# Kernel tuning notes

Hardware: AMD Instinct MI355X
Metric: run time of the kernel (lower is better)

## Reference

```python
import jax, jax.numpy as jnp
import numpy as np

B, S, E, H, D = 1, 2048, 1024, 16, 64
LAM_INIT = 0.8  # \u03bbinit from init_kwargs
LN_EPS = 1e-5


def setup_inputs() -> dict:
    key = jax.random.key(0)
    ks = jax.random.split(key, 6)
    w = 0.02  # weight init scale
    return {
        "X": jax.random.normal(ks[0], (B, S, E), dtype=jnp.float32),
        "Wq": jax.random.normal(ks[1], (H, E, 2 * D), dtype=jnp.float32) * w,
        "bq": jnp.zeros((H, 2 * D), dtype=jnp.float32),
        "Wk": jax.random.normal(ks[2], (H, E, 2 * D), dtype=jnp.float32) * w,
        "bk": jnp.zeros((H, 2 * D), dtype=jnp.float32),
        "Wv": jax.random.normal(ks[3], (H, E, D), dtype=jnp.float32) * w,
        "bv": jnp.zeros((H, D), dtype=jnp.float32),
        "Wo": jax.random.normal(ks[4], (H * D, E), dtype=jnp.float32) * w,
        "bo": jnp.zeros((E,), dtype=jnp.float32),
        "gamma": jnp.ones((E,), dtype=jnp.float32),
        "beta": jnp.zeros((E,), dtype=jnp.float32),
        "lam": jnp.float32(0.5),
    }


def reference(X, Wq, bq, Wk, bk, Wv, bv, Wo, bo, gamma, beta, lam):
    # Batched over heads: Q,K -> [B,H,S,2D], V -> [B,H,S,D]
    Q = jnp.einsum("bse,hec->bhsc", X, Wq) + bq[None, :, None, :]
    K = jnp.einsum("bse,hec->bhsc", X, Wk) + bk[None, :, None, :]
    V = jnp.einsum("bse,hed->bhsd", X, Wv) + bv[None, :, None, :]
    d = Wv.shape[-1]
    Q1, Q2 = Q[..., :d], Q[..., d:]
    K1, K2 = K[..., :d], K[..., d:]
    s = 1.0 / jnp.sqrt(jnp.float32(d))
    A1 = jnp.einsum("bhqd,bhkd->bhqk", Q1, K1) * s
    A2 = jnp.einsum("bhqd,bhkd->bhqk", Q2, K2) * s
    P = jax.nn.softmax(A1, axis=-1) - lam * jax.nn.softmax(A2, axis=-1)
    O = jnp.einsum("bhqk,bhkd->bhqd", P, V)  # [B,H,S,D]
    Ocat = jnp.transpose(O, (0, 2, 1, 3)).reshape(O.shape[0], O.shape[2], -1)  # [B,S,H*D]
    Y = Ocat @ Wo + bo
    mu = jnp.mean(Y, axis=-1, keepdims=True)
    var = jnp.var(Y, axis=-1, keepdims=True)
    Yn = (Y - mu) * jax.lax.rsqrt(var + LN_EPS) * gamma + beta
    return Yn * (1.0 - LAM_INIT)
```

## Files before the change

kernel.cpp:

```cpp
#include <hip/hip_runtime.h>

#define S_LEN 2048
#define EDIM  1024
#define HEADS 16
#define DHEAD 64

typedef __attribute__((ext_vector_type(8))) short bf16x8;
typedef __attribute__((ext_vector_type(4))) short short4v;
typedef __attribute__((ext_vector_type(4))) float f32x4;

__device__ inline unsigned short f2bf(float f) {
    unsigned int u = __float_as_uint(f);
    unsigned int r = (u + 0x7FFFu + ((u >> 16) & 1u)) >> 16;
    return (unsigned short)r;
}
__device__ inline float bf2f(unsigned short b) {
    return __uint_as_float(((unsigned int)b) << 16);
}
__device__ inline void load_lds16(const void* g, void* l) {
    __builtin_amdgcn_global_load_lds(
        (const __attribute__((address_space(1))) unsigned int*)g,
        (__attribute__((address_space(3))) unsigned int*)l, 16, 0, 0);
}

__global__ void k_convert_x(const float* __restrict__ x, short* __restrict__ xb, int n4) {
    int i = blockIdx.x * blockDim.x + threadIdx.x;
    if (i >= n4) return;
    f32x4 v = ((const f32x4*)x)[i];
    short4v o;
    o[0] = (short)f2bf(v[0]); o[1] = (short)f2bf(v[1]);
    o[2] = (short)f2bf(v[2]); o[3] = (short)f2bf(v[3]);
    ((short4v*)xb)[i] = o;
}

__global__ void k_transpose_cvt(const float* __restrict__ in, short* __restrict__ out, int R, int C) {
    __shared__ float tile[32][33];
    const int b = blockIdx.z;
    in  += (size_t)b * R * C;
    out += (size_t)b * R * C;
    const int c0 = blockIdx.x * 32, r0 = blockIdx.y * 32;
    #pragma unroll
    for (int yy = 0; yy < 4; ++yy) {
        int r = r0 + threadIdx.y + yy * 8, c = c0 + threadIdx.x;
        tile[threadIdx.y + yy * 8][threadIdx.x] = (r < R && c < C) ? in[(size_t)r * C + c] : 0.f;
    }
    __syncthreads();
    #pragma unroll
    for (int yy = 0; yy < 4; ++yy) {
        int c = c0 + threadIdx.y + yy * 8, r = r0 + threadIdx.x;
        if (c < C && r < R) out[(size_t)c * R + r] = (short)f2bf(tile[threadIdx.x][threadIdx.y + yy * 8]);
    }
}

template<int BM, int BN, int WR, int WC>
__device__ inline void gemm_core(const char* Ag, int ldaB, const char* Bg, int ldbB,
                                 int K, char* sA, char* sB, f32x4* acc) {
    constexpr int FM = BM / (WR * 16), FN = BN / (WC * 16);
    constexpr int RA = BM / 32, RB = BN / 32;
    const int lane = threadIdx.x & 63, wave = threadIdx.x >> 6;
    const int rl = lane & 15, g = lane >> 4;
    const int wrow = (wave / WC) * (BM / WR);
    const int wcol = (wave % WC) * (BN / WC);
    const int lr = lane >> 3;
    const int lc = ((lane & 7) ^ lr) << 4;
    const char* aSrc = Ag + (size_t)(wave * 8 + lr) * ldaB + lc;
    const char* bSrc = Bg + (size_t)(wave * 8 + lr) * ldbB + lc;

    for (int t = 0; t < K / 64; ++t) {
        __syncthreads();
        #pragma unroll
        for (int i = 0; i < RA; ++i)
            load_lds16(aSrc + (size_t)t * 128 + (size_t)i * 32 * ldaB, sA + (i * 4 + wave) * 1024);
        #pragma unroll
        for (int i = 0; i < RB; ++i)
            load_lds16(bSrc + (size_t)t * 128 + (size_t)i * 32 * ldbB, sB + (i * 4 + wave) * 1024);
        __syncthreads();
        #pragma unroll
        for (int kk = 0; kk < 2; ++kk) {
            bf16x8 af[FM], bf[FN];
            #pragma unroll
            for (int f = 0; f < FM; ++f) {
                const int r = wrow + f * 16 + rl;
                af[f] = *(const bf16x8*)(sA + r * 128 + (((kk * 4 + g) ^ (r & 7)) << 4));
            }
            #pragma unroll
            for (int j = 0; j < FN; ++j) {
                const int r = wcol + j * 16 + rl;
                bf[j] = *(const bf16x8*)(sB + r * 128 + (((kk * 4 + g) ^ (r & 7)) << 4));
            }
            #pragma unroll
            for (int f = 0; f < FM; ++f)
                #pragma unroll
                for (int j = 0; j < FN; ++j)
                    acc[f * FN + j] = __builtin_amdgcn_mfma_f32_16x16x32_bf16(af[f], bf[j], acc[f * FN + j], 0, 0, 0);
        }
    }
}

__global__ __launch_bounds__(256) void k_gemm_qkv(
        const short* __restrict__ Xb,
        const short* __restrict__ WqT, const short* __restrict__ WkT, const short* __restrict__ WvT,
        const float* __restrict__ bq, const float* __restrict__ bk, const float* __restrict__ bv,
        short* __restrict__ Qh, short* __restrict__ Kh, short* __restrict__ Vt) {
    __shared__ __align__(16) char sA[16384], sB[16384];
    int id = blockIdx.x;
    id = (id & 7) * 80 + (id >> 3);
    const int mbase = (id % 16) * 128;
    const int y = id / 16;

    const short* Bt; const float* bias; int nbase; int which;
    if (y < 16)      { which = 0; Bt = WqT; bias = bq; nbase = y * 128; }
    else if (y < 32) { which = 1; Bt = WkT; bias = bk; nbase = (y - 16) * 128; }
    else             { which = 2; Bt = WvT; bias = bv; nbase = (y - 32) * 128; }

    f32x4 acc[16];
    #pragma unroll
    for (int i = 0; i < 16; ++i) acc[i] = (f32x4){0.f, 0.f, 0.f, 0.f};

    gemm_core<128, 128, 2, 2>((const char*)Xb + (size_t)mbase * 2048, 2048,
                              (const char*)Bt + (size_t)nbase * 2048, 2048,
                              EDIM, sA, sB, acc);

    const int lane = threadIdx.x & 63, wave = threadIdx.x >> 6;
    const int wr = (wave >> 1) * 64, wc = (wave & 1) * 64;
    const int rl = lane & 15, g = lane >> 4;
    const float qscale = 0.125f * 1.44269504088896f;
    #pragma unroll
    for (int i = 0; i < 4; ++i)
        #pragma unroll
        for (int j = 0; j < 4; ++j)
            #pragma unroll
            for (int jj = 0; jj < 4; ++jj) {
                int s = mbase + wr + i * 16 + g * 4 + jj;
                int n = nbase + wc + j * 16 + rl;
                float v = acc[i * 4 + j][jj] + bias[n];
                if (which == 0) v *= qscale;
                short b16 = (short)f2bf(v);
                if (which == 0)      Qh[((size_t)(n >> 7) * S_LEN + s) * 128 + (n & 127)] = b16;
                else if (which == 1) Kh[((size_t)(n >> 7) * S_LEN + s) * 128 + (n & 127)] = b16;
                else                 Vt[(size_t)n * S_LEN + s] = b16;
            }
}

__global__ __launch_bounds__(256) void k_attn(
        const short* __restrict__ Qh, const short* __restrict__ Kh,
        const short* __restrict__ Vt, const float* __restrict__ lam_p,
        short* __restrict__ Ocat) {
    __shared__ __align__(16) char smem[65536];
    char* Kl = smem;
    char* Vl = smem + 32768;
    char* Pl = smem + 49152;

    const int lane = threadIdx.x & 63, wave = threadIdx.x >> 6;
    const int rl = lane & 15, g = lane >> 4;
    const int h = blockIdx.y;
    const int qbase = blockIdx.x * 64 + wave * 16;
    const int swz = (rl & 7) << 4;
    const int kx = rl & 7;

    const char* Kgb = (const char*)(Kh + (size_t)h * S_LEN * 128);
    const char* Vgb = (const char*)(Vt + (size_t)h * DHEAD * S_LEN);
    const short* Qp = Qh + (size_t)h * S_LEN * 128;
    char* Pb0 = Pl + wave * 4096;
    char* Pb1 = Pb0 + 2048;

    const int kofs0 = (lane >> 4) * 256 + (((lane & 15) ^ (lane >> 4)) << 4);
    const int kofs1 = (lane >> 4) * 256 + (((lane & 15) ^ ((lane >> 4) + 4)) << 4);
    const int vofs  = (lane >> 3) * 4096 + (((lane & 7) ^ (lane >> 3)) << 4);

    bf16x8 qf[2][2];
    #pragma unroll
    for (int p = 0; p < 2; ++p)
        #pragma unroll
        for (int kc = 0; kc < 2; ++kc)
            qf[p][kc] = *(const bf16x8*)&Qp[(size_t)(qbase + rl) * 128 + p * 64 + kc * 32 + g * 8];

    #pragma unroll
    for (int cc = 0; cc < 4; ++cc) {
        int c = wave * 4 + cc;
        load_lds16(Kgb + c * 1024 + ((cc & 1) ? kofs1 : kofs0), Kl + c * 1024);
    }
    #pragma unroll
    for (int cc = 0; cc < 2; ++cc) {
        int c = wave * 2 + cc;
        load_lds16(Vgb + (size_t)c * 32768 + vofs, Vl + c * 1024);
    }

    f32x4 acc[2][4];
    float m[2], l[2];
    #pragma unroll
    for (int p = 0; p < 2; ++p) {
        #pragma unroll
        for (int t = 0; t < 4; ++t) acc[p][t] = (f32x4){0.f, 0.f, 0.f, 0.f};
        m[p] = 0.f; l[p] = 0.f;
    }

    __syncthreads();

    const int NIT = S_LEN / 64;
    for (int it = 0; it < NIT; ++it) {
        const int cur = it & 1;
        if (it + 1 < NIT) {
            const size_t nkv = (size_t)(it + 1) * 64;
            char* kb = Kl + (cur ^ 1) * 16384;
            char* vb = Vl + (cur ^ 1) * 8192;
            #pragma unroll
            for (int cc = 0; cc < 4; ++cc) {
                int c = wave * 4 + cc;
                load_lds16(Kgb + nkv * 256 + c * 1024 + ((cc & 1) ? kofs1 : kofs0), kb + c * 1024);
            }
            #pragma unroll
            for (int cc = 0; cc < 2; ++cc) {
                int c = wave * 2 + cc;
                load_lds16(Vgb + (size_t)c * 32768 + nkv * 2 + vofs, vb + c * 1024);
            }
        }
        const char* kb = Kl + cur * 16384;
        const char* vb = Vl + cur * 8192;

        f32x4 sc[2][4];
        #pragma unroll
        for (int t = 0; t < 4; ++t) {
            #pragma unroll
            for (int p = 0; p < 2; ++p) {
                f32x4 z = (f32x4){0.f, 0.f, 0.f, 0.f};
                #pragma unroll
                for (int kc = 0; kc < 2; ++kc) {
                    bf16x8 kf = *(const bf16x8*)(kb + t * 4096 + rl * 256 + (((p * 8 + kc * 4 + g) ^ kx) << 4));
                    z = __builtin_amdgcn_mfma_f32_16x16x32_bf16(kf, qf[p][kc], z, 0, 0, 0);
                }
                sc[p][t] = z;
            }
        }

        float bm[2];
        #pragma unroll
        for (int p = 0; p < 2; ++p) {
            float mx = sc[p][0][0];
            #pragma unroll
            for (int t = 0; t < 4; ++t)
                #pragma unroll
                for (int jj = 0; jj < 4; ++jj)
                    mx = fmaxf(mx, sc[p][t][jj]);
            mx = fmaxf(mx, __shfl_xor(mx, 16, 64));
            mx = fmaxf(mx, __shfl_xor(mx, 32, 64));
            bm[p] = mx;
        }

        if (it == 0) {
            m[0] = bm[0]; m[1] = bm[1];
        } else if (!__all((bm[0] <= m[0] + 8.f) && (bm[1] <= m[1] + 8.f))) {
            #pragma unroll
            for (int p = 0; p < 2; ++p) {
                float mn = fmaxf(m[p], bm[p]);
                float fac = exp2f(m[p] - mn);
                l[p] *= fac; m[p] = mn;
                #pragma unroll
                for (int jj = 0; jj < 4; ++jj) {
                    float fq = __shfl(fac, g * 4 + jj, 64);
                    #pragma unroll
                    for (int t = 0; t < 4; ++t) acc[p][t][jj] *= fq;
                }
            }
        }

        #pragma unroll
        for (int p = 0; p < 2; ++p) {
            char* Pb = p ? Pb1 : Pb0;
            float rs = 0.f;
            #pragma unroll
            for (int t = 0; t < 4; ++t) {
                #pragma unroll
                for (int jjp = 0; jjp < 4; jjp += 2) {
                    float e0 = exp2f(sc[p][t][jjp]     - m[p]);
                    float e1 = exp2f(sc[p][t][jjp + 1] - m[p]);
                    rs += e0 + e1;
                    unsigned u;
                    asm("v_cvt_pk_bf16_f32 %0, %1, %2" : "=v"(u) : "v"(e0), "v"(e1));
                    *(unsigned*)(Pb + rl * 128 + (((t * 16 + g * 4 + jjp) * 2) ^ swz)) = u;
                }
            }
            rs += __shfl_xor(rs, 16, 64);
            rs += __shfl_xor(rs, 32, 64);
            l[p] += rs;
        }

        #pragma unroll
        for (int kc = 0; kc < 2; ++kc) {
            bf16x8 pa0 = *(const bf16x8*)(Pb0 + rl * 128 + ((kc * 64 + g * 16) ^ swz));
            bf16x8 pa1 = *(const bf16x8*)(Pb1 + rl * 128 + ((kc * 64 + g * 16) ^ swz));
            #pragma unroll
            for (int t = 0; t < 4; ++t) {
                bf16x8 vf = *(const bf16x8*)(vb + t * 2048 + rl * 128 + (((kc * 4 + g) ^ kx) << 4));
                acc[0][t] = __builtin_amdgcn_mfma_f32_16x16x32_bf16(pa0, vf, acc[0][t], 0, 0, 0);
                acc[1][t] = __builtin_amdgcn_mfma_f32_16x16x32_bf16(pa1, vf, acc[1][t], 0, 0, 0);
            }
        }
        __syncthreads();
    }

    const float lam = lam_p[0];
    float inv0[4], inv1[4];
    #pragma unroll
    for (int jj = 0; jj < 4; ++jj) {
        inv0[jj] = 1.0f / __shfl(l[0], g * 4 + jj, 64);
        inv1[jj] = lam  / __shfl(l[1], g * 4 + jj, 64);
    }
    #pragma unroll
    for (int t = 0; t < 4; ++t)
        #pragma unroll
        for (int jj = 0; jj < 4; ++jj) {
            float o = acc[0][t][jj] * inv0[jj] - acc[1][t][jj] * inv1[jj];
            int s = qbase + g * 4 + jj;
            Ocat[(size_t)s * 1024 + h * 64 + t * 16 + rl] = (short)f2bf(o);
        }
}

__global__ __launch_bounds__(256) void k_gemm_out(
        const short* __restrict__ Ocat, const short* __restrict__ WoT,
        const float* __restrict__ bo, float* __restrict__ Yws) {
    __shared__ __align__(16) char sA[8192], sB[16384];
    int id = blockIdx.x;
    id = (id & 7) * 32 + (id >> 3);
    const int mbase = (id % 32) * 64;
    const int nbase = (id / 32) * 128;

    f32x4 acc[8];
    #pragma unroll
    for (int i = 0; i < 8; ++i) acc[i] = (f32x4){0.f, 0.f, 0.f, 0.f};

    gemm_core<64, 128, 1, 4>((const char*)Ocat + (size_t)mbase * 2048, 2048,
                             (const char*)WoT + (size_t)nbase * 2048, 2048,
                             1024, sA, sB, acc);

    const int lane = threadIdx.x & 63, wave = threadIdx.x >> 6;
    const int rl = lane & 15, g = lane >> 4;
    #pragma unroll
    for (int f = 0; f < 4; ++f)
        #pragma unroll
        for (int j = 0; j < 2; ++j)
            #pragma unroll
            for (int jj = 0; jj < 4; ++jj) {
                int s = mbase + f * 16 + g * 4 + jj;
                int e = nbase + wave * 32 + j * 16 + rl;
                Yws[(size_t)s * 1024 + e] = acc[f * 2 + j][jj] + bo[e];
            }
}

__global__ __launch_bounds__(256) void k_ln(
        const float* __restrict__ Yws, const float* __restrict__ gamma,
        const float* __restrict__ beta, float* __restrict__ out) {
    const int s = blockIdx.x;
    const int tid = threadIdx.x;
    f32x4 y = ((const f32x4*)(Yws + (size_t)s * 1024))[tid];
    float sum = y[0] + y[1] + y[2] + y[3];
    float sq  = y[0]*y[0] + y[1]*y[1] + y[2]*y[2] + y[3]*y[3];
    #pragma unroll
    for (int off = 1; off < 64; off <<= 1) {
        sum += __shfl_xor(sum, off, 64);
        sq  += __shfl_xor(sq,  off, 64);
    }
    __shared__ float ls[2][4];
    const int wave = tid >> 6, lane = tid & 63;
    if (lane == 0) { ls[0][wave] = sum; ls[1][wave] = sq; }
    __syncthreads();
    sum = ls[0][0] + ls[0][1] + ls[0][2] + ls[0][3];
    sq  = ls[1][0] + ls[1][1] + ls[1][2] + ls[1][3];
    const float mu = sum * (1.f / 1024.f);
    const float var = sq * (1.f / 1024.f) - mu * mu;
    const float rstd = rsqrtf(var + 1e-5f);
    f32x4 gg = ((const f32x4*)gamma)[tid];
    f32x4 bb = ((const f32x4*)beta)[tid];
    f32x4 o;
    #pragma unroll
    for (int k = 0; k < 4; ++k)
        o[k] = ((y[k] - mu) * rstd * gg[k] + bb[k]) * 0.2f;
    ((f32x4*)(out + (size_t)s * 1024))[tid] = o;
}

extern "C" void kernel_launch(void* const* d_in, const int* in_sizes, int n_in,
                              void* d_out, int out_size, void* d_ws, size_t ws_size,
                              hipStream_t stream) {
    const float* X     = (const float*)d_in[0];
    const float* Wq    = (const float*)d_in[1];
    const float* bq    = (const float*)d_in[2];
    const float* Wk    = (const float*)d_in[3];
    const float* bk    = (const float*)d_in[4];
    const float* Wv    = (const float*)d_in[5];
    const float* bv    = (const float*)d_in[6];
    const float* Wo    = (const float*)d_in[7];
    const float* bo    = (const float*)d_in[8];
    const float* gamma = (const float*)d_in[9];
    const float* beta  = (const float*)d_in[10];
    const float* lam   = (const float*)d_in[11];
    float* out = (float*)d_out;

    char* ws = (char*)d_ws;
    const size_t MB = 1u << 20;
    short* Xb  = (short*)(ws + 0);
    short* WqT = (short*)(ws + 4 * MB);
    short* WkT = (short*)(ws + 8 * MB);
    short* WvT = (short*)(ws + 12 * MB);
    short* WoT = (short*)(ws + 14 * MB);
    short* Qh  = (short*)(ws + 16 * MB);
    short* Kh  = (short*)(ws + 24 * MB);
    short* Vt  = (short*)(ws + 32 * MB);
    short* Oc  = (short*)(ws + 36 * MB);
    float* Yws = (float*)(ws + 0);

    k_convert_x<<<dim3(2048), dim3(256), 0, stream>>>(X, Xb, (S_LEN * EDIM) / 4);
    k_transpose_cvt<<<dim3(4, 32, 16), dim3(32, 8), 0, stream>>>(Wq, WqT, 1024, 128);
    k_transpose_cvt<<<dim3(4, 32, 16), dim3(32, 8), 0, stream>>>(Wk, WkT, 1024, 128);
    k_transpose_cvt<<<dim3(2, 32, 16), dim3(32, 8), 0, stream>>>(Wv, WvT, 1024, 64);
    k_transpose_cvt<<<dim3(32, 32, 1), dim3(32, 8), 0, stream>>>(Wo, WoT, 1024, 1024);
    k_gemm_qkv<<<dim3(640), dim3(256), 0, stream>>>(Xb, WqT, WkT, WvT, bq, bk, bv, Qh, Kh, Vt);
    k_attn<<<dim3(32, 16), dim3(256), 0, stream>>>(Qh, Kh, Vt, lam, Oc);
    k_gemm_out<<<dim3(256), dim3(256), 0, stream>>>(Oc, WoT, bo, Yws);
    k_ln<<<dim3(2048), dim3(256), 0, stream>>>(Yws, gamma, beta, out);
}
```

Measured before the change: 178.1 us.

## Split attention KV range across two wave groups with LDS merge

The attention kernel now launches 512 threads per block. Two groups of four waves each process half of the key/value sequence for the same 64 queries. The partial outputs, maxima and sums are merged through LDS in a flash-decoding style combine. KV double-buffered prefetch is replaced by synchronous load-then-compute with two barriers per iteration, and the two softmax branches are processed sequentially to reduce register pressure. The aim is more waves per CU to hide latency, at the cost of losing load/compute overlap, adding a merge step, and storing the partial accumulators as bf16.

```diff
diff --git a/kernel.cpp b/kernel.cpp
--- a/kernel.cpp
+++ b/kernel.cpp
@@ -142,27 +142,27 @@
             }
 }
 
-__global__ __launch_bounds__(256) void k_attn(
+__global__ __launch_bounds__(512, 4) void k_attn(
         const short* __restrict__ Qh, const short* __restrict__ Kh,
         const short* __restrict__ Vt, const float* __restrict__ lam_p,
         short* __restrict__ Ocat) {
     __shared__ __align__(16) char smem[65536];
-    char* Kl = smem;
-    char* Vl = smem + 32768;
-    char* Pl = smem + 49152;
 
     const int lane = threadIdx.x & 63, wave = threadIdx.x >> 6;
     const int rl = lane & 15, g = lane >> 4;
+    const int qw = wave & 3, kvg = wave >> 2;
     const int h = blockIdx.y;
-    const int qbase = blockIdx.x * 64 + wave * 16;
+    const int qbase = blockIdx.x * 64 + qw * 16;
     const int swz = (rl & 7) << 4;
     const int kx = rl & 7;
+
+    char* Kl = smem + kvg * 16384;
+    char* Vl = smem + 32768 + kvg * 8192;
+    char* Pw = smem + 49152 + wave * 2048;
 
     const char* Kgb = (const char*)(Kh + (size_t)h * S_LEN * 128);
     const char* Vgb = (const char*)(Vt + (size_t)h * DHEAD * S_LEN);
     const short* Qp = Qh + (size_t)h * S_LEN * 128;
-    char* Pb0 = Pl + wave * 4096;
-    char* Pb1 = Pb0 + 2048;
 
     const int kofs0 = (lane >> 4) * 256 + (((lane & 15) ^ (lane >> 4)) << 4);
     const int kofs1 = (lane >> 4) * 256 + (((lane & 15) ^ ((lane >> 4) + 4)) << 4);
@@ -175,17 +175,6 @@
         for (int kc = 0; kc < 2; ++kc)
             qf[p][kc] = *(const bf16x8*)&Qp[(size_t)(qbase + rl) * 128 + p * 64 + kc * 32 + g * 8];
 
-    #pragma unroll
-    for (int cc = 0; cc < 4; ++cc) {
-        int c = wave * 4 + cc;
-        load_lds16(Kgb + c * 1024 + ((cc & 1) ? kofs1 : kofs0), Kl + c * 1024);
-    }
-    #pragma unroll
-    for (int cc = 0; cc < 2; ++cc) {
-        int c = wave * 2 + cc;
-        load_lds16(Vgb + (size_t)c * 32768 + vofs, Vl + c * 1024);
-    }
-
     f32x4 acc[2][4];
     float m[2], l[2];
     #pragma unroll
@@ -195,64 +184,49 @@
         m[p] = 0.f; l[p] = 0.f;
     }
 
-    __syncthreads();
-
-    const int NIT = S_LEN / 64;
+    const int NIT = 1024 / 64;
     for (int it = 0; it < NIT; ++it) {
-        const int cur = it & 1;
-        if (it + 1 < NIT) {
-            const size_t nkv = (size_t)(it + 1) * 64;
-            char* kb = Kl + (cur ^ 1) * 16384;
-            char* vb = Vl + (cur ^ 1) * 8192;
-            #pragma unroll
-            for (int cc = 0; cc < 4; ++cc) {
-                int c = wave * 4 + cc;
-                load_lds16(Kgb + nkv * 256 + c * 1024 + ((cc & 1) ? kofs1 : kofs0), kb + c * 1024);
-            }
-            #pragma unroll
-            for (int cc = 0; cc < 2; ++cc) {
-                int c = wave * 2 + cc;
-                load_lds16(Vgb + (size_t)c * 32768 + nkv * 2 + vofs, vb + c * 1024);
-            }
-        }
-        const char* kb = Kl + cur * 16384;
-        const char* vb = Vl + cur * 8192;
-
-        f32x4 sc[2][4];
-        #pragma unroll
-        for (int t = 0; t < 4; ++t) {
-            #pragma unroll
-            for (int p = 0; p < 2; ++p) {
+        const size_t kv0 = (size_t)(kvg * 1024 + it * 64);
+        __syncthreads();
+        #pragma unroll
+        for (int cc = 0; cc < 4; ++cc) {
+            int c = qw * 4 + cc;
+            load_lds16(Kgb + kv0 * 256 + c * 1024 + ((cc & 1) ? kofs1 : kofs0), Kl + c * 1024);
+        }
+        #pragma unroll
+        for (int cc = 0; cc < 2; ++cc) {
+            int c = qw * 2 + cc;
+            load_lds16(Vgb + (size_t)c * 32768 + kv0 * 2 + vofs, Vl + c * 1024);
+        }
+        __syncthreads();
+
+        #pragma unroll
+        for (int p = 0; p < 2; ++p) {
+            f32x4 sc[4];
+            #pragma unroll
+            for (int t = 0; t < 4; ++t) {
                 f32x4 z = (f32x4){0.f, 0.f, 0.f, 0.f};
                 #pragma unroll
                 for (int kc = 0; kc < 2; ++kc) {
-                    bf16x8 kf = *(const bf16x8*)(kb + t * 4096 + rl * 256 + (((p * 8 + kc * 4 + g) ^ kx) << 4));
+                    bf16x8 kf = *(const bf16x8*)(Kl + t * 4096 + rl * 256 + (((p * 8 + kc * 4 + g) ^ kx) << 4));
                     z = __builtin_amdgcn_mfma_f32_16x16x32_bf16(kf, qf[p][kc], z, 0, 0, 0);
                 }
-                sc[p][t] = z;
-            }
-        }
-
-        float bm[2];
-        #pragma unroll
-        for (int p = 0; p < 2; ++p) {
-            float mx = sc[p][0][0];
+                sc[t] = z;
+            }
+
+            float mx = sc[0][0];
             #pragma unroll
             for (int t = 0; t < 4; ++t)
                 #pragma unroll
                 for (int jj = 0; jj < 4; ++jj)
-                    mx = fmaxf(mx, sc[p][t][jj]);
+                    mx = fmaxf(mx, sc[t][jj]);
             mx = fmaxf(mx, __shfl_xor(mx, 16, 64));
             mx = fmaxf(mx, __shfl_xor(mx, 32, 64));
-            bm[p] = mx;
-        }
-
-        if (it == 0) {
-            m[0] = bm[0]; m[1] = bm[1];
-        } else if (!__all((bm[0] <= m[0] + 8.f) && (bm[1] <= m[1] + 8.f))) {
-            #pragma unroll
-            for (int p = 0; p < 2; ++p) {
-                float mn = fmaxf(m[p], bm[p]);
+
+            if (it == 0) {
+                m[p] = mx;
+            } else if (!__all(mx <= m[p] + 8.f)) {
+                float mn = fmaxf(m[p], mx);
                 float fac = exp2f(m[p] - mn);
                 l[p] *= fac; m[p] = mn;
                 #pragma unroll
@@ -262,58 +236,81 @@
                     for (int t = 0; t < 4; ++t) acc[p][t][jj] *= fq;
                 }
             }
-        }
-
-        #pragma unroll
-        for (int p = 0; p < 2; ++p) {
-            char* Pb = p ? Pb1 : Pb0;
+
             float rs = 0.f;
             #pragma unroll
             for (int t = 0; t < 4; ++t) {
                 #pragma unroll
                 for (int jjp = 0; jjp < 4; jjp += 2) {
-                    float e0 = exp2f(sc[p][t][jjp]     - m[p]);
-                    float e1 = exp2f(sc[p][t][jjp + 1] - m[p]);
+                    float e0 = exp2f(sc[t][jjp]     - m[p]);
+                    float e1 = exp2f(sc[t][jjp + 1] - m[p]);
                     rs += e0 + e1;
                     unsigned u;
                     asm("v_cvt_pk_bf16_f32 %0, %1, %2" : "=v"(u) : "v"(e0), "v"(e1));
-                    *(unsigned*)(Pb + rl * 128 + (((t * 16 + g * 4 + jjp) * 2) ^ swz)) = u;
+                    *(unsigned*)(Pw + rl * 128 + (((t * 16 + g * 4 + jjp) * 2) ^ swz)) = u;
                 }
             }
             rs += __shfl_xor(rs, 16, 64);
             rs += __shfl_xor(rs, 32, 64);
             l[p] += rs;
-        }
-
-        #pragma unroll
-        for (int kc = 0; kc < 2; ++kc) {
-            bf16x8 pa0 = *(const bf16x8*)(Pb0 + rl * 128 + ((kc * 64 + g * 16) ^ swz));
-            bf16x8 pa1 = *(const bf16x8*)(Pb1 + rl * 128 + ((kc * 64 + g * 16) ^ swz));
-            #pragma unroll
-            for (int t = 0; t < 4; ++t) {
-                bf16x8 vf = *(const bf16x8*)(vb + t * 2048 + rl * 128 + (((kc * 4 + g) ^ kx) << 4));
-                acc[0][t] = __builtin_amdgcn_mfma_f32_16x16x32_bf16(pa0, vf, acc[0][t], 0, 0, 0);
-                acc[1][t] = __builtin_amdgcn_mfma_f32_16x16x32_bf16(pa1, vf, acc[1][t], 0, 0, 0);
-            }
-        }
-        __syncthreads();
-    }
-
-    const float lam = lam_p[0];
-    float inv0[4], inv1[4];
-    #pragma unroll
-    for (int jj = 0; jj < 4; ++jj) {
-        inv0[jj] = 1.0f / __shfl(l[0], g * 4 + jj, 64);
-        inv1[jj] = lam  / __shfl(l[1], g * 4 + jj, 64);
-    }
-    #pragma unroll
-    for (int t = 0; t < 4; ++t)
-        #pragma unroll
-        for (int jj = 0; jj < 4; ++jj) {
-            float o = acc[0][t][jj] * inv0[jj] - acc[1][t][jj] * inv1[jj];
-            int s = qbase + g * 4 + jj;
-            Ocat[(size_t)s * 1024 + h * 64 + t * 16 + rl] = (short)f2bf(o);
-        }
+
+            #pragma unroll
+            for (int kc = 0; kc < 2; ++kc) {
+                bf16x8 pa = *(const bf16x8*)(Pw + rl * 128 + ((kc * 64 + g * 16) ^ swz));
+                #pragma unroll
+                for (int t = 0; t < 4; ++t) {
+                    bf16x8 vf = *(const bf16x8*)(Vl + t * 2048 + rl * 128 + (((kc * 4 + g) ^ kx) << 4));
+                    acc[p][t] = __builtin_amdgcn_mfma_f32_16x16x32_bf16(pa, vf, acc[p][t], 0, 0, 0);
+                }
+            }
+        }
+    }
+
+    __syncthreads();
+    {
+        unsigned short* Xw = (unsigned short*)(smem + wave * 4096);
+        float* ML = (float*)(smem + 32768);
+        #pragma unroll
+        for (int p = 0; p < 2; ++p) {
+            #pragma unroll
+            for (int t = 0; t < 4; ++t)
+                #pragma unroll
+                for (int jj = 0; jj < 4; ++jj)
+                    Xw[p * 1024 + (g * 4 + jj) * 64 + t * 16 + rl] = f2bf(acc[p][t][jj]);
+            if (g == 0) {
+                ML[(wave * 2 + p) * 32 + rl]      = m[p];
+                ML[(wave * 2 + p) * 32 + 16 + rl] = l[p];
+            }
+        }
+    }
+    __syncthreads();
+
+    {
+        const int q = threadIdx.x >> 3, d0 = (threadIdx.x & 7) * 8;
+        const int q15 = q & 15, wa = q >> 4, wb = (q >> 4) + 4;
+        const float* ML = (const float*)(smem + 32768);
+        const float lam = lam_p[0];
+        float res[2][8];
+        float invL[2];
+        #pragma unroll
+        for (int p = 0; p < 2; ++p) {
+            float ma = ML[(wa * 2 + p) * 32 + q15], la = ML[(wa * 2 + p) * 32 + 16 + q15];
+            float mb = ML[(wb * 2 + p) * 32 + q15], lb = ML[(wb * 2 + p) * 32 + 16 + q15];
+            float ms = fmaxf(ma, mb);
+            float fa = exp2f(ma - ms), fb = exp2f(mb - ms);
+            invL[p] = 1.0f / (fa * la + fb * lb);
+            const unsigned short* xa = (const unsigned short*)(smem + wa * 4096 + p * 2048 + q15 * 128 + d0 * 2);
+            const unsigned short* xb = (const unsigned short*)(smem + wb * 4096 + p * 2048 + q15 * 128 + d0 * 2);
+            #pragma unroll
+            for (int k = 0; k < 8; ++k)
+                res[p][k] = fa * bf2f(xa[k]) + fb * bf2f(xb[k]);
+        }
+        bf16x8 ov;
+        #pragma unroll
+        for (int k = 0; k < 8; ++k)
+            ov[k] = (short)f2bf(res[0][k] * invL[0] - lam * res[1][k] * invL[1]);
+        *(bf16x8*)&Ocat[(size_t)(blockIdx.x * 64 + q) * 1024 + h * 64 + d0] = ov;
+    }
 }
 
 __global__ __launch_bounds__(256) void k_gemm_out(
@@ -414,7 +411,7 @@
     k_transpose_cvt<<<dim3(2, 32, 16), dim3(32, 8), 0, stream>>>(Wv, WvT, 1024, 64);
     k_transpose_cvt<<<dim3(32, 32, 1), dim3(32, 8), 0, stream>>>(Wo, WoT, 1024, 1024);
     k_gemm_qkv<<<dim3(640), dim3(256), 0, stream>>>(Xb, WqT, WkT, WvT, bq, bk, bv, Qh, Kh, Vt);
-    k_attn<<<dim3(32, 16), dim3(256), 0, stream>>>(Qh, Kh, Vt, lam, Oc);
+    k_attn<<<dim3(32, 16), dim3(512), 0, stream>>>(Qh, Kh, Vt, lam, Oc);
     k_gemm_out<<<dim3(256), dim3(256), 0, stream>>>(Oc, WoT, bo, Yws);
     k_ln<<<dim3(2048), dim3(256), 0, stream>>>(Yws, gamma, beta, out);
 }
```

Measured after the change: 173.1 us (median of 2 runs). 1.03x faster.
